# Optimization experiments

Measured on AMD Instinct MI355X. Metric: run time of the kernel, lower is better.

Reference implementation:

```python
import jax, jax.numpy as jnp
import numpy as np

B, U, E = 4, 8192, 128
GH, GW = 64, 64
S = GH * GW
H = 8
DH = E // H
MAX_PATCH = 24  # static bucket cap: max off-grid tokens per cell + 1 grid/fake slot


def setup_inputs() -> dict:
    key = jax.random.key(0)
    ks = jax.random.split(key, 9)
    xc_off_grid = jax.random.uniform(ks[0], (B, U, 2), dtype=jnp.float32)
    gy = jnp.linspace(0.0, 1.0, GH)
    gx = jnp.linspace(0.0, 1.0, GW)
    grid = jnp.stack(jnp.meshgrid(gy, gx, indexing="ij"), axis=-1)  # [GH, GW, 2]
    xc_on_grid = jnp.broadcast_to(grid, (B, GH, GW, 2))
    zc_off_grid = jax.random.normal(ks[1], (B, U, E), dtype=jnp.float32)
    zc_on_grid = jax.random.normal(ks[2], (B, GH, GW, E), dtype=jnp.float32)
    latents = jax.random.normal(ks[3], (GH, GW, E), dtype=jnp.float32)
    fake_embedding = jax.random.normal(ks[4], (E,), dtype=jnp.float32)
    sc = 1.0 / np.sqrt(E).astype(np.float32)
    Wq = jax.random.normal(ks[5], (E, E), dtype=jnp.float32) * sc
    Wk = jax.random.normal(ks[6], (E, E), dtype=jnp.float32) * sc
    Wv = jax.random.normal(ks[7], (E, E), dtype=jnp.float32) * sc
    Wo = jax.random.normal(ks[8], (E, E), dtype=jnp.float32) * sc
    return dict(xc_off_grid=xc_off_grid, xc_on_grid=xc_on_grid,
                zc_off_grid=zc_off_grid, zc_on_grid=zc_on_grid,
                latents=latents, fake_embedding=fake_embedding,
                Wq=Wq, Wk=Wk, Wv=Wv, Wo=Wo, ignore_on_grid=0)


def _nearest_flat_idx(x, x_grid):
    # uniform grid -> nearest cell via per-dim rounding (matches the repo's
    # nearest_gridded_neighbours with k=1 on a regular grid)
    ax0 = x_grid[0, :, 0, 0]  # [GH] coords along dim 0
    ax1 = x_grid[0, 0, :, 1]  # [GW] coords along dim 1
    i0 = jnp.clip(jnp.round((x[..., 0] - ax0[0]) / (ax0[1] - ax0[0])), 0, GH - 1).astype(jnp.int32)
    i1 = jnp.clip(jnp.round((x[..., 1] - ax1[0]) / (ax1[1] - ax1[0])), 0, GW - 1).astype(jnp.int32)
    return i0 * GW + i1  # [B, U]


def _bucketize(nearest):
    # flat bucket id per off-grid token + rank of the token within its bucket
    # (rank in ascending u order, matching torch's cumsum-based cumcount_idx)
    flat = (jnp.arange(B, dtype=jnp.int32)[:, None] * S + nearest).reshape(-1)  # [B*U]
    order = jnp.argsort(flat)  # stable sort -> preserves u order within a bucket
    sf = flat[order]
    pos = jnp.arange(B * U, dtype=jnp.int32)
    is_start = jnp.concatenate([jnp.ones((1,), bool), sf[1:] != sf[:-1]])
    start = jax.lax.cummax(jnp.where(is_start, pos, 0), axis=0)
    cumcount = jnp.zeros(B * U, jnp.int32).at[order].set(pos - start)
    counts = jax.ops.segment_sum(jnp.ones(B * U, jnp.int32), flat, num_segments=B * S)
    return flat, cumcount, counts


def reference(xc_off_grid, xc_on_grid, zc_off_grid, zc_on_grid,
              latents, fake_embedding, Wq, Wk, Wv, Wo, ignore_on_grid):
    nearest = _nearest_flat_idx(xc_off_grid, xc_on_grid)  # [B, U]
    flat, cumcount, counts = _bucketize(nearest)
    counts = jnp.minimum(counts, MAX_PATCH - 1)

    # scatter off-grid tokens into per-cell buckets (slot MAX_PATCH-1 reserved)
    slot = jnp.where(cumcount >= MAX_PATCH - 1, MAX_PATCH, cumcount)  # overflow -> dropped
    z_flat = zc_off_grid.reshape(B * U, E)
    grid_stacked = jnp.zeros((B * S, MAX_PATCH, E), zc_off_grid.dtype)
    grid_stacked = grid_stacked.at[flat, slot].set(z_flat, mode="drop")

    if ignore_on_grid:
        last = jnp.broadcast_to(fake_embedding, (B * S, E))
    else:
        last = zc_on_grid.reshape(B * S, E)
    grid_stacked = grid_stacked.at[:, -1].set(last)

    p = jnp.arange(MAX_PATCH)
    valid = (p[None, :] < counts[:, None]) | (p[None, :] == MAX_PATCH - 1)  # [B*S, P]

    # single-query masked multi-head cross-attention per grid cell
    lat = jnp.broadcast_to(latents.reshape(1, S, E), (B, S, E)).reshape(B * S, E)
    q = (lat @ Wq).reshape(B * S, H, DH)
    k = (grid_stacked @ Wk).reshape(B * S, MAX_PATCH, H, DH)
    v = (grid_stacked @ Wv).reshape(B * S, MAX_PATCH, H, DH)
    scores = jnp.einsum("nhd,nphd->nhp", q, k) / np.sqrt(DH).astype(np.float32)
    scores = jnp.where(valid[:, None, :], scores, -jnp.inf)
    attn = jax.nn.softmax(scores, axis=-1)
    out = jnp.einsum("nhp,nphd->nhd", attn, v).reshape(B * S, E) @ Wo
    return out.reshape(B, GH, GW, E)  # z_grid (xc_on_grid passthrough omitted)
```

## Files before the change

kernel.cpp:

```cpp
#include <hip/hip_runtime.h>
#include <hip/hip_bf16.h>
#include <math.h>

#define BB    4
#define UU    8192
#define EE    128
#define GH_   64
#define GW_   64
#define SS    (GH_ * GW_)
#define KEEP  23
#define MSTRIDE 24
#define OFFROWS (BB * UU)
#define NROWS   (BB * UU + BB * SS)
#define POISON  0xAAAAAAAAu
#define NKV     768
#define BKT0    NKV
#define WTO0    (NKV + 64)
#define Q0      (NKV + 68)
#define D1GRID  (NKV + 100)

typedef short bf16x8 __attribute__((ext_vector_type(8)));
typedef float f32x4  __attribute__((ext_vector_type(4)));

__device__ inline short f2bf(float f) {
    unsigned u = __float_as_uint(f);
    u += 0x7FFF + ((u >> 16) & 1);
    return (short)(u >> 16);
}
__device__ inline unsigned xor1(unsigned v) {
    return (unsigned)__builtin_amdgcn_mov_dpp((int)v, 0xB1, 0xF, 0xF, true);
}

#define OFF_COUNTS  0
#define OFF_MEMBERS 65536
#define OFF_WTO     1638400
#define OFF_QB      1671168
#define OFF_KV      3768320

__global__ __launch_bounds__(512) void d1_kernel(
    const float* __restrict__ xc,
    const float* __restrict__ zc_off, const float* __restrict__ zc_on,
    const float* __restrict__ fake, const int* __restrict__ ignore_flag,
    const float* __restrict__ Wk, const float* __restrict__ Wv,
    const float* __restrict__ Wo, const float* __restrict__ Wq,
    const float* __restrict__ latents,
    unsigned* __restrict__ counts, int* __restrict__ members,
    short* __restrict__ WtO, float* __restrict__ Qb,
    unsigned* __restrict__ KVb32)
{
    __shared__ __align__(16) short shWt[16384];
    const int blk  = blockIdx.x;
    const int tid  = threadIdx.x;

    if (blk < NKV) {
        const int wave = tid >> 6;
        const int lane = tid & 63;
        const int m16  = lane & 15;
        const int quad = lane >> 4;
        const bool isV = blk & 1;
        const int unit = blk >> 1;
        const float* W = isV ? Wv : Wk;
        unsigned* dst  = KVb32 + (isV ? 64 : 0);

        unsigned* WtL32 = (unsigned*)shWt;
        #pragma unroll
        for (int it = 0; it < 16; ++it) {
            int idx = tid + it * 512;
            int n  = idx & 127;
            int kh = idx >> 7;
            unsigned lo = (unsigned short)f2bf(W[(2 * kh)     * EE + n]);
            unsigned hi = (unsigned short)f2bf(W[(2 * kh + 1) * EE + n]);
            WtL32[(kh >> 2) * 512 + n * 4 + (kh & 3)] = lo | (hi << 16);
        }
        __syncthreads();

        const int row0 = unit * 128 + wave * 16;
        const int mrow = row0 + m16;
        const float* src;
        if (mrow < OFFROWS)    src = zc_off + (size_t)mrow * EE;
        else if (*ignore_flag) src = fake;
        else                   src = zc_on + (size_t)(mrow - OFFROWS) * EE;

        bf16x8 afrag[4];
        #pragma unroll
        for (int ks = 0; ks < 4; ++ks) {
            int k0 = ks * 32 + quad * 8;
            float4 a0 = *(const float4*)(src + k0);
            float4 a1 = *(const float4*)(src + k0 + 4);
            bf16x8 f;
            f[0] = f2bf(a0.x); f[1] = f2bf(a0.y); f[2] = f2bf(a0.z); f[3] = f2bf(a0.w);
            f[4] = f2bf(a1.x); f[5] = f2bf(a1.y); f[6] = f2bf(a1.z); f[7] = f2bf(a1.w);
            afrag[ks] = f;
        }

        f32x4 acc[8];
        #pragma unroll
        for (int ct = 0; ct < 8; ++ct) acc[ct] = (f32x4)(0.f);

        #pragma unroll
        for (int ct = 0; ct < 8; ++ct) {
            const int n = ct * 16 + m16;
            #pragma unroll
            for (int ks = 0; ks < 4; ++ks) {
                const int kc = ks * 4 + quad;
                bf16x8 w = *(const bf16x8*)(shWt + kc * 1024 + n * 8);
                acc[ct] = __builtin_amdgcn_mfma_f32_16x16x32_bf16(afrag[ks], w, acc[ct], 0, 0, 0);
            }
        }

        const int rsel = (m16 & 1) * 2;
        #pragma unroll
        for (int ct = 0; ct < 8; ++ct) {
            unsigned dw[4];
            #pragma unroll
            for (int r = 0; r < 4; ++r) {
                unsigned my = (unsigned short)f2bf(acc[ct][r]);
                unsigned ot = xor1(my);
                dw[r] = (m16 & 1) ? (ot | (my << 16)) : (my | (ot << 16));
            }
            const int cidx = ct * 8 + (m16 >> 1);
            #pragma unroll
            for (int rr = 0; rr < 2; ++rr) {
                const int row = row0 + quad * 4 + rsel + rr;
                dst[(size_t)row * 128 + cidx] = dw[rsel + rr];
            }
        }
    } else if (blk < WTO0) {
        int i = (blk - BKT0) * 512 + tid;
        int b = i >> 13;
        float x0 = xc[2 * i + 0];
        float x1 = xc[2 * i + 1];
        const float step = 1.0f / 63.0f;
        int i0 = (int)rintf(x0 / step);
        i0 = min(max(i0, 0), GH_ - 1);
        int i1 = (int)rintf(x1 / step);
        i1 = min(max(i1, 0), GW_ - 1);
        int bucket = b * SS + i0 * GW_ + i1;
        int slot = (int)(atomicAdd(&counts[bucket], 1u) - POISON);
        if (slot < KEEP) members[bucket * MSTRIDE + slot] = i;
    } else if (blk < Q0) {
        short (*T)[130] = (short(*)[130])shWt;
        const int p = blk - WTO0;
        #pragma unroll
        for (int j = 0; j < 8; ++j) {
            int idx = tid + j * 512;
            int kk = idx >> 7, n = idx & 127;
            T[kk][n] = f2bf(Wo[(p * 32 + kk) * EE + n]);
        }
        __syncthreads();
        unsigned* Wt32 = (unsigned*)WtO;
        #pragma unroll
        for (int j = 0; j < 4; ++j) {
            int idx = tid + j * 512;
            int n = idx >> 4, ku = idx & 15;
            unsigned lo = (unsigned short)T[2 * ku][n];
            unsigned hi = (unsigned short)T[2 * ku + 1][n];
            Wt32[n * 64 + p * 16 + ku] = lo | (hi << 16);
        }
    } else {
        const int wave = tid >> 6;
        const int lane = tid & 63;
        const int m16  = lane & 15;
        const int quad = lane >> 4;
        const int row0 = ((blk - Q0) * 8 + wave) * 16;
        const float* src = latents + (size_t)(row0 + m16) * EE;

        bf16x8 afrag[4];
        #pragma unroll
        for (int ks = 0; ks < 4; ++ks) {
            int k0 = ks * 32 + quad * 8;
            float4 a0 = *(const float4*)(src + k0);
            float4 a1 = *(const float4*)(src + k0 + 4);
            bf16x8 f;
            f[0] = f2bf(a0.x); f[1] = f2bf(a0.y); f[2] = f2bf(a0.z); f[3] = f2bf(a0.w);
            f[4] = f2bf(a1.x); f[5] = f2bf(a1.y); f[6] = f2bf(a1.z); f[7] = f2bf(a1.w);
            afrag[ks] = f;
        }

        f32x4 acc[8];
        #pragma unroll
        for (int ct = 0; ct < 8; ++ct) acc[ct] = (f32x4)(0.f);
        #pragma unroll
        for (int ct = 0; ct < 8; ++ct) {
            const int n = ct * 16 + m16;
            #pragma unroll
            for (int ks = 0; ks < 4; ++ks) {
                const int k0 = ks * 32 + quad * 8;
                bf16x8 w;
                #pragma unroll
                for (int j = 0; j < 8; ++j)
                    w[j] = f2bf(Wq[(size_t)(k0 + j) * EE + n]);
                acc[ct] = __builtin_amdgcn_mfma_f32_16x16x32_bf16(afrag[ks], w, acc[ct], 0, 0, 0);
            }
        }
        #pragma unroll
        for (int ct = 0; ct < 8; ++ct) {
            #pragma unroll
            for (int r = 0; r < 4; ++r)
                Qb[(size_t)(row0 + quad * 4 + r) * EE + ct * 16 + m16] = acc[ct][r];
        }
    }
}

__global__ __launch_bounds__(256) void attn_wo_kernel(
    const float* __restrict__ Qb,
    const unsigned* __restrict__ KVb32,
    const unsigned* __restrict__ counts,
    const int*  __restrict__ members,
    const short* __restrict__ WtO,
    float* __restrict__ out)
{
    __shared__ float At[16][132];
    const int tid  = threadIdx.x;
    const int wave = tid >> 6;
    const int lane = tid & 63;
    const int b0   = blockIdx.x * 16;
    const int bw   = b0 + wave * 4;

    int4 cnt4r = *(const int4*)&counts[bw];
    int cnt[4] = { (int)((unsigned)cnt4r.x - POISON),
                   (int)((unsigned)cnt4r.y - POISON),
                   (int)((unsigned)cnt4r.z - POISON),
                   (int)((unsigned)cnt4r.w - POISON) };
    int4   m4[4];
    float2 q[4];
    #pragma unroll
    for (int i = 0; i < 4; ++i) {
        cnt[i] = min(max(cnt[i], 0), KEEP);
        m4[i] = *(const int4*)&members[(bw + i) * MSTRIDE];
        q[i]  = *(const float2*)(Qb + (size_t)((bw + i) & (SS - 1)) * EE + 2 * lane);
    }

    unsigned kuA[4][5], vuA[4][5];
    #pragma unroll
    for (int i = 0; i < 4; ++i) {
        const int ongrid = OFFROWS + bw + i;
        const int c = cnt[i];
        int rows[5];
        rows[0] = (0 < c) ? m4[i].x : ongrid;
        rows[1] = (1 < c) ? m4[i].y : ongrid;
        rows[2] = (2 < c) ? m4[i].z : ongrid;
        rows[3] = (3 < c) ? m4[i].w : ongrid;
        rows[4] = ongrid;
        #pragma unroll
        for (int p = 0; p < 5; ++p) {
            const unsigned* kvrow = KVb32 + (size_t)rows[p] * 128;
            kuA[i][p] = kvrow[lane];
            vuA[i][p] = kvrow[64 + lane];
        }
    }

    #pragma unroll
    for (int i = 0; i < 4; ++i) {
        const int bucket = bw + i;
        const int c = cnt[i];

        float sc[5]; float2 vv[5];
        #pragma unroll
        for (int p = 0; p < 5; ++p) {
            unsigned ku = kuA[i][p];
            unsigned vu = vuA[i][p];
            float kx = __uint_as_float(ku << 16);
            float ky = __uint_as_float(ku & 0xFFFF0000u);
            vv[p].x  = __uint_as_float(vu << 16);
            vv[p].y  = __uint_as_float(vu & 0xFFFF0000u);
            float pr = q[i].x * kx + q[i].y * ky;
            pr += __shfl_xor(pr, 1);
            pr += __shfl_xor(pr, 2);
            pr += __shfl_xor(pr, 4);
            sc[p] = (p < c || p == 4) ? pr * 0.25f : -INFINITY;
        }
        float m = sc[4];
        #pragma unroll
        for (int p = 0; p < 4; ++p) m = fmaxf(m, sc[p]);
        float l = 0.f, ox = 0.f, oy = 0.f;
        #pragma unroll
        for (int p = 0; p < 5; ++p) {
            float w = __expf(sc[p] - m);
            l += w;
            ox += w * vv[p].x;
            oy += w * vv[p].y;
        }
        for (int p = 4; p < c; ++p) {
            int row = members[bucket * MSTRIDE + p];
            const unsigned* kvrow = KVb32 + (size_t)row * 128;
            unsigned ku = kvrow[lane];
            unsigned vu = kvrow[64 + lane];
            float kx = __uint_as_float(ku << 16);
            float ky = __uint_as_float(ku & 0xFFFF0000u);
            float vx = __uint_as_float(vu << 16);
            float vy = __uint_as_float(vu & 0xFFFF0000u);
            float pr = q[i].x * kx + q[i].y * ky;
            pr += __shfl_xor(pr, 1);
            pr += __shfl_xor(pr, 2);
            pr += __shfl_xor(pr, 4);
            float s  = pr * 0.25f;
            float mn = fmaxf(m, s);
            float al = __expf(m - mn);
            float w  = __expf(s - mn);
            l  = l * al + w;
            ox = ox * al + w * vx;
            oy = oy * al + w * vy;
            m  = mn;
        }
        float inv = 1.0f / l;
        *(float2*)(&At[wave * 4 + i][2 * lane]) = make_float2(ox * inv, oy * inv);
    }
    __syncthreads();

    const int m16  = lane & 15;
    const int quad = lane >> 4;

    bf16x8 afrag[4];
    #pragma unroll
    for (int ks = 0; ks < 4; ++ks) {
        const float* arow = &At[m16][ks * 32 + quad * 8];
        float4 a0 = *(const float4*)(arow);
        float4 a1 = *(const float4*)(arow + 4);
        bf16x8 f;
        f[0] = f2bf(a0.x); f[1] = f2bf(a0.y); f[2] = f2bf(a0.z); f[3] = f2bf(a0.w);
        f[4] = f2bf(a1.x); f[5] = f2bf(a1.y); f[6] = f2bf(a1.z); f[7] = f2bf(a1.w);
        afrag[ks] = f;
    }

    f32x4 acc[2];
    acc[0] = (f32x4)(0.f); acc[1] = (f32x4)(0.f);
    #pragma unroll
    for (int c = 0; c < 2; ++c) {
        const int ct = wave * 2 + c;
        #pragma unroll
        for (int ks = 0; ks < 4; ++ks) {
            const int woff = (ct * 16 + m16) * EE + ks * 32 + quad * 8;
            bf16x8 w = *(const bf16x8*)(WtO + woff);
            acc[c] = __builtin_amdgcn_mfma_f32_16x16x32_bf16(afrag[ks], w, acc[c], 0, 0, 0);
        }
    }
    #pragma unroll
    for (int c = 0; c < 2; ++c) {
        #pragma unroll
        for (int r = 0; r < 4; ++r)
            out[(size_t)(b0 + quad * 4 + r) * EE + (wave * 2 + c) * 16 + m16] = acc[c][r];
    }
}

extern "C" void kernel_launch(void* const* d_in, const int* in_sizes, int n_in,
                              void* d_out, int out_size, void* d_ws, size_t ws_size,
                              hipStream_t stream)
{
    const float* xc_off  = (const float*)d_in[0];
    const float* zc_off  = (const float*)d_in[2];
    const float* zc_on   = (const float*)d_in[3];
    const float* latents = (const float*)d_in[4];
    const float* fake    = (const float*)d_in[5];
    const float* Wq      = (const float*)d_in[6];
    const float* Wk      = (const float*)d_in[7];
    const float* Wv      = (const float*)d_in[8];
    const float* Wo      = (const float*)d_in[9];
    const int*   ignore  = (const int*)d_in[10];

    char* ws = (char*)d_ws;
    unsigned* counts  = (unsigned*)(ws + OFF_COUNTS);
    int*      members = (int*)(ws + OFF_MEMBERS);
    short*    WtO     = (short*)(ws + OFF_WTO);
    float*    Qb      = (float*)(ws + OFF_QB);
    unsigned* KVb     = (unsigned*)(ws + OFF_KV);
    float*    outp    = (float*)d_out;

    d1_kernel<<<D1GRID, 512, 0, stream>>>(
        xc_off, zc_off, zc_on, fake, ignore,
        Wk, Wv, Wo, Wq, latents,
        counts, members, WtO, Qb, KVb);

    attn_wo_kernel<<<BB * SS / 16, 256, 0, stream>>>(
        Qb, KVb, counts, members, WtO, outp);
}
```

Measured before the change: 125.6 us.

## Fuse K/V projection per block and stage Wq in LDS for Q projection

Each K/V block now computes both the K and V projections for its 128 rows, reusing the A fragments and staging both bf16 weight matrices in LDS with vectorized float4 loads. This halves the number of K/V blocks and the repeated activation loads. The Q projection also stages Wq in LDS instead of doing strided scalar global reads, and its blocks are reordered ahead of bucketing. In the attention kernel the on-grid K/V row loads are issued before the counts are decoded, so they can overlap with the member index loads. In exchange, LDS use doubles to 64 KB per block, which can lower occupancy, and each K/V block keeps two accumulator sets live, which raises register pressure.

```diff
diff --git a/kernel.cpp b/kernel.cpp
--- a/kernel.cpp
+++ b/kernel.cpp
@@ -13,11 +13,12 @@
 #define OFFROWS (BB * UU)
 #define NROWS   (BB * UU + BB * SS)
 #define POISON  0xAAAAAAAAu
-#define NKV     768
-#define BKT0    NKV
-#define WTO0    (NKV + 64)
-#define Q0      (NKV + 68)
-#define D1GRID  (NKV + 100)
+#define KV0     0
+#define NKV     384
+#define Q0      384
+#define BKT0    416
+#define WTO0    480
+#define D1GRID  484
 
 typedef short bf16x8 __attribute__((ext_vector_type(8)));
 typedef float f32x4  __attribute__((ext_vector_type(4)));
@@ -26,6 +27,9 @@
     unsigned u = __float_as_uint(f);
     u += 0x7FFF + ((u >> 16) & 1);
     return (short)(u >> 16);
+}
+__device__ inline unsigned packbf(float lo, float hi) {
+    return (unsigned)(unsigned short)f2bf(lo) | ((unsigned)(unsigned short)f2bf(hi) << 16);
 }
 __device__ inline unsigned xor1(unsigned v) {
     return (unsigned)__builtin_amdgcn_mov_dpp((int)v, 0xB1, 0xF, 0xF, true);
@@ -36,6 +40,25 @@
 #define OFF_WTO     1638400
 #define OFF_QB      1671168
 #define OFF_KV      3768320
+
+__device__ inline void stage_w(const float* __restrict__ W, unsigned* WtL32,
+                               int matOff, int tid)
+{
+    #pragma unroll
+    for (int c = 0; c < 4; ++c) {
+        int idx = tid + c * 512;
+        int n4 = idx & 31, kh = idx >> 5;
+        const float* r0 = W + (2 * kh) * EE + 4 * n4;
+        float4 f0 = *(const float4*)r0;
+        float4 f1 = *(const float4*)(r0 + EE);
+        int kc = kh >> 2, kd = kh & 3;
+        unsigned base = matOff + kc * 512 + (4 * n4) * 4 + kd;
+        WtL32[base + 0]  = packbf(f0.x, f1.x);
+        WtL32[base + 4]  = packbf(f0.y, f1.y);
+        WtL32[base + 8]  = packbf(f0.z, f1.z);
+        WtL32[base + 12] = packbf(f0.w, f1.w);
+    }
+}
 
 __global__ __launch_bounds__(512) void d1_kernel(
     const float* __restrict__ xc,
@@ -48,33 +71,21 @@
     short* __restrict__ WtO, float* __restrict__ Qb,
     unsigned* __restrict__ KVb32)
 {
-    __shared__ __align__(16) short shWt[16384];
+    __shared__ __align__(16) short shWt[32768];
     const int blk  = blockIdx.x;
     const int tid  = threadIdx.x;
+    const int wave = tid >> 6;
+    const int lane = tid & 63;
+    const int m16  = lane & 15;
+    const int quad = lane >> 4;
 
     if (blk < NKV) {
-        const int wave = tid >> 6;
-        const int lane = tid & 63;
-        const int m16  = lane & 15;
-        const int quad = lane >> 4;
-        const bool isV = blk & 1;
-        const int unit = blk >> 1;
-        const float* W = isV ? Wv : Wk;
-        unsigned* dst  = KVb32 + (isV ? 64 : 0);
-
         unsigned* WtL32 = (unsigned*)shWt;
-        #pragma unroll
-        for (int it = 0; it < 16; ++it) {
-            int idx = tid + it * 512;
-            int n  = idx & 127;
-            int kh = idx >> 7;
-            unsigned lo = (unsigned short)f2bf(W[(2 * kh)     * EE + n]);
-            unsigned hi = (unsigned short)f2bf(W[(2 * kh + 1) * EE + n]);
-            WtL32[(kh >> 2) * 512 + n * 4 + (kh & 3)] = lo | (hi << 16);
-        }
+        stage_w(Wk, WtL32, 0,    tid);
+        stage_w(Wv, WtL32, 8192, tid);
         __syncthreads();
 
-        const int row0 = unit * 128 + wave * 16;
+        const int row0 = blk * 128 + wave * 16;
         const int mrow = row0 + m16;
         const float* src;
         if (mrow < OFFROWS)    src = zc_off + (size_t)mrow * EE;
@@ -93,10 +104,67 @@
             afrag[ks] = f;
         }
 
+        f32x4 acc1[8], acc2[8];
+        #pragma unroll
+        for (int ct = 0; ct < 8; ++ct) { acc1[ct] = (f32x4)(0.f); acc2[ct] = (f32x4)(0.f); }
+
+        #pragma unroll
+        for (int ct = 0; ct < 8; ++ct) {
+            const int n = ct * 16 + m16;
+            #pragma unroll
+            for (int ks = 0; ks < 4; ++ks) {
+                const int kc = ks * 4 + quad;
+                bf16x8 w1 = *(const bf16x8*)(shWt + kc * 1024 + n * 8);
+                acc1[ct] = __builtin_amdgcn_mfma_f32_16x16x32_bf16(afrag[ks], w1, acc1[ct], 0, 0, 0);
+                bf16x8 w2 = *(const bf16x8*)(shWt + 16384 + kc * 1024 + n * 8);
+                acc2[ct] = __builtin_amdgcn_mfma_f32_16x16x32_bf16(afrag[ks], w2, acc2[ct], 0, 0, 0);
+            }
+        }
+
+        const int rsel = (m16 & 1) * 2;
+        #pragma unroll
+        for (int ct = 0; ct < 8; ++ct) {
+            unsigned dw1[4], dw2[4];
+            #pragma unroll
+            for (int r = 0; r < 4; ++r) {
+                unsigned my1 = (unsigned short)f2bf(acc1[ct][r]);
+                unsigned ot1 = xor1(my1);
+                dw1[r] = (m16 & 1) ? (ot1 | (my1 << 16)) : (my1 | (ot1 << 16));
+                unsigned my2 = (unsigned short)f2bf(acc2[ct][r]);
+                unsigned ot2 = xor1(my2);
+                dw2[r] = (m16 & 1) ? (ot2 | (my2 << 16)) : (my2 | (ot2 << 16));
+            }
+            const int cidx = ct * 8 + (m16 >> 1);
+            #pragma unroll
+            for (int rr = 0; rr < 2; ++rr) {
+                const int row = row0 + quad * 4 + rsel + rr;
+                KVb32[(size_t)row * 128 + cidx]      = dw1[rsel + rr];
+                KVb32[(size_t)row * 128 + 64 + cidx] = dw2[rsel + rr];
+            }
+        }
+    } else if (blk < BKT0) {
+        unsigned* WtL32 = (unsigned*)shWt;
+        stage_w(Wq, WtL32, 0, tid);
+        __syncthreads();
+
+        const int row0 = (blk - Q0) * 128 + wave * 16;
+        const float* src = latents + (size_t)(row0 + m16) * EE;
+
+        bf16x8 afrag[4];
+        #pragma unroll
+        for (int ks = 0; ks < 4; ++ks) {
+            int k0 = ks * 32 + quad * 8;
+            float4 a0 = *(const float4*)(src + k0);
+            float4 a1 = *(const float4*)(src + k0 + 4);
+            bf16x8 f;
+            f[0] = f2bf(a0.x); f[1] = f2bf(a0.y); f[2] = f2bf(a0.z); f[3] = f2bf(a0.w);
+            f[4] = f2bf(a1.x); f[5] = f2bf(a1.y); f[6] = f2bf(a1.z); f[7] = f2bf(a1.w);
+            afrag[ks] = f;
+        }
+
         f32x4 acc[8];
         #pragma unroll
         for (int ct = 0; ct < 8; ++ct) acc[ct] = (f32x4)(0.f);
-
         #pragma unroll
         for (int ct = 0; ct < 8; ++ct) {
             const int n = ct * 16 + m16;
@@ -107,23 +175,11 @@
                 acc[ct] = __builtin_amdgcn_mfma_f32_16x16x32_bf16(afrag[ks], w, acc[ct], 0, 0, 0);
             }
         }
-
-        const int rsel = (m16 & 1) * 2;
         #pragma unroll
         for (int ct = 0; ct < 8; ++ct) {
-            unsigned dw[4];
-            #pragma unroll
-            for (int r = 0; r < 4; ++r) {
-                unsigned my = (unsigned short)f2bf(acc[ct][r]);
-                unsigned ot = xor1(my);
-                dw[r] = (m16 & 1) ? (ot | (my << 16)) : (my | (ot << 16));
-            }
-            const int cidx = ct * 8 + (m16 >> 1);
-            #pragma unroll
-            for (int rr = 0; rr < 2; ++rr) {
-                const int row = row0 + quad * 4 + rsel + rr;
-                dst[(size_t)row * 128 + cidx] = dw[rsel + rr];
-            }
+            #pragma unroll
+            for (int r = 0; r < 4; ++r)
+                Qb[(size_t)(row0 + quad * 4 + r) * EE + ct * 16 + m16] = acc[ct][r];
         }
     } else if (blk < WTO0) {
         int i = (blk - BKT0) * 512 + tid;
@@ -138,7 +194,7 @@
         int bucket = b * SS + i0 * GW_ + i1;
         int slot = (int)(atomicAdd(&counts[bucket], 1u) - POISON);
         if (slot < KEEP) members[bucket * MSTRIDE + slot] = i;
-    } else if (blk < Q0) {
+    } else {
         short (*T)[130] = (short(*)[130])shWt;
         const int p = blk - WTO0;
         #pragma unroll
@@ -156,48 +212,6 @@
             unsigned lo = (unsigned short)T[2 * ku][n];
             unsigned hi = (unsigned short)T[2 * ku + 1][n];
             Wt32[n * 64 + p * 16 + ku] = lo | (hi << 16);
-        }
-    } else {
-        const int wave = tid >> 6;
-        const int lane = tid & 63;
-        const int m16  = lane & 15;
-        const int quad = lane >> 4;
-        const int row0 = ((blk - Q0) * 8 + wave) * 16;
-        const float* src = latents + (size_t)(row0 + m16) * EE;
-
-        bf16x8 afrag[4];
-        #pragma unroll
-        for (int ks = 0; ks < 4; ++ks) {
-            int k0 = ks * 32 + quad * 8;
-            float4 a0 = *(const float4*)(src + k0);
-            float4 a1 = *(const float4*)(src + k0 + 4);
-            bf16x8 f;
-            f[0] = f2bf(a0.x); f[1] = f2bf(a0.y); f[2] = f2bf(a0.z); f[3] = f2bf(a0.w);
-            f[4] = f2bf(a1.x); f[5] = f2bf(a1.y); f[6] = f2bf(a1.z); f[7] = f2bf(a1.w);
-            afrag[ks] = f;
-        }
-
-        f32x4 acc[8];
-        #pragma unroll
-        for (int ct = 0; ct < 8; ++ct) acc[ct] = (f32x4)(0.f);
-        #pragma unroll
-        for (int ct = 0; ct < 8; ++ct) {
-            const int n = ct * 16 + m16;
-            #pragma unroll
-            for (int ks = 0; ks < 4; ++ks) {
-                const int k0 = ks * 32 + quad * 8;
-                bf16x8 w;
-                #pragma unroll
-                for (int j = 0; j < 8; ++j)
-                    w[j] = f2bf(Wq[(size_t)(k0 + j) * EE + n]);
-                acc[ct] = __builtin_amdgcn_mfma_f32_16x16x32_bf16(afrag[ks], w, acc[ct], 0, 0, 0);
-            }
-        }
-        #pragma unroll
-        for (int ct = 0; ct < 8; ++ct) {
-            #pragma unroll
-            for (int r = 0; r < 4; ++r)
-                Qb[(size_t)(row0 + quad * 4 + r) * EE + ct * 16 + m16] = acc[ct][r];
         }
     }
 }
@@ -218,32 +232,35 @@
     const int bw   = b0 + wave * 4;
 
     int4 cnt4r = *(const int4*)&counts[bw];
+    unsigned kuA[4][5], vuA[4][5];
+    int4   m4[4];
+    float2 q[4];
+    #pragma unroll
+    for (int i = 0; i < 4; ++i) {
+        const unsigned* kvrow = KVb32 + (size_t)(OFFROWS + bw + i) * 128;
+        kuA[i][4] = kvrow[lane];
+        vuA[i][4] = kvrow[64 + lane];
+        m4[i] = *(const int4*)&members[(bw + i) * MSTRIDE];
+        q[i]  = *(const float2*)(Qb + (size_t)((bw + i) & (SS - 1)) * EE + 2 * lane);
+    }
     int cnt[4] = { (int)((unsigned)cnt4r.x - POISON),
                    (int)((unsigned)cnt4r.y - POISON),
                    (int)((unsigned)cnt4r.z - POISON),
                    (int)((unsigned)cnt4r.w - POISON) };
-    int4   m4[4];
-    float2 q[4];
-    #pragma unroll
-    for (int i = 0; i < 4; ++i) {
-        cnt[i] = min(max(cnt[i], 0), KEEP);
-        m4[i] = *(const int4*)&members[(bw + i) * MSTRIDE];
-        q[i]  = *(const float2*)(Qb + (size_t)((bw + i) & (SS - 1)) * EE + 2 * lane);
-    }
-
-    unsigned kuA[4][5], vuA[4][5];
+    #pragma unroll
+    for (int i = 0; i < 4; ++i) cnt[i] = min(max(cnt[i], 0), KEEP);
+
     #pragma unroll
     for (int i = 0; i < 4; ++i) {
         const int ongrid = OFFROWS + bw + i;
         const int c = cnt[i];
-        int rows[5];
+        int rows[4];
         rows[0] = (0 < c) ? m4[i].x : ongrid;
         rows[1] = (1 < c) ? m4[i].y : ongrid;
         rows[2] = (2 < c) ? m4[i].z : ongrid;
         rows[3] = (3 < c) ? m4[i].w : ongrid;
-        rows[4] = ongrid;
-        #pragma unroll
-        for (int p = 0; p < 5; ++p) {
+        #pragma unroll
+        for (int p = 0; p < 4; ++p) {
             const unsigned* kvrow = KVb32 + (size_t)rows[p] * 128;
             kuA[i][p] = kvrow[lane];
             vuA[i][p] = kvrow[64 + lane];
```

Result: faster. 117.0 us (-6.8%).
